# Kernel tuning notes

Hardware: AMD Instinct MI355X
Metric: run time of the kernel (lower is better)

Reference implementation:

```python
import jax, jax.numpy as jnp
import numpy as np
from jax import lax

B, K = 16, 10
C_IN, C_OUT = 32, 64
H_IN, W_IN = 32, 32
KS, STRIDE, PAD = 3, 1, 1
H_OUT = (H_IN + 2 * PAD - KS) // STRIDE + 1
W_OUT = (W_IN + 2 * PAD - KS) // STRIDE + 1


def setup_inputs() -> dict:
    key = jax.random.key(0)
    k1, k2, k3 = jax.random.split(key, 3)
    x = jax.random.normal(k1, (B, K, C_IN, H_IN, W_IN), dtype=jnp.float32)
    # init_local (non-mono, non-first): std = 1/sqrt(0.5 * in_ch * k^2)
    std = 1.0 / np.sqrt(0.5 * C_IN * KS ** 2)
    weight = jax.random.normal(k2, (H_OUT, W_OUT, C_OUT, C_IN, KS, KS), dtype=jnp.float32) * std
    bias = jax.random.normal(k3, (K, C_OUT, H_OUT, W_OUT), dtype=jnp.float32) * 0.01
    return {"x": x, "weight": weight, "bias": bias}


def reference(x, weight, bias):
    # x: [B, K, C_in, H, W] -> merge batch and category dims
    b, k = x.shape[:2]
    xr = x.reshape((b * k,) + x.shape[2:])  # [BK, C_in, H, W]
    # Extract all kxk patches in one fused op: [BK, C_in*KS*KS, h_out, w_out]
    # feature dim ordered (c, kh, kw) -- matches weight layout [o, i, kh, kw].
    patches = lax.conv_general_dilated_patches(
        xr, filter_shape=(KS, KS), window_strides=(STRIDE, STRIDE),
        padding=[(PAD, PAD), (PAD, PAD)])
    w2 = weight.reshape(H_OUT, W_OUT, C_OUT, C_IN * KS * KS)  # [i, j, o, f]
    # Per-pixel unshared contraction (block-diagonal batched GEMM)
    out = jnp.einsum('bfij,ijof->boij', patches, w2)  # [BK, C_out, h_out, w_out]
    out = out.reshape(b, k, C_OUT, H_OUT, W_OUT)
    return out + bias[None]
```

## Files before the change

### kernel.cpp

```cpp
#include <hip/hip_runtime.h>


#define HW    32
#define CIN   32
#define COUT  64
#define FDIM  288
#define FPAD  296
#define NBK   160
#define HP    34
#define PLANE (NBK * CIN)

using f32x4  = __attribute__((ext_vector_type(4))) float;
using bf16x8 = __attribute__((ext_vector_type(8))) short;
using s16x4  = __attribute__((ext_vector_type(4))) short;

static __device__ inline unsigned short f2bf(float f) {
    unsigned u = __float_as_uint(f);
    u += 0x7FFFu + ((u >> 16) & 1u);
    return (unsigned short)(u >> 16);
}
static constexpr size_t XC_BYTES = (size_t)HP * HP * PLANE * 2;
static constexpr size_t CO_BYTES = (size_t)1024 * COUT * NBK * 2;

__global__ __launch_bounds__(256) void hz_kernel(short* __restrict__ xc)
{
    const int id = blockIdx.x;
    int h, w;
    if (id < 34)      { h = 0;  w = id; }
    else if (id < 68) { h = 33; w = id - 34; }
    else { const int e = id - 68; h = 1 + (e >> 1); w = (e & 1) * 33; }
    uint2* p = reinterpret_cast<uint2*>(xc + (size_t)(h * HP + w) * PLANE);
    const uint2 z = {0u, 0u};
#pragma unroll
    for (int r = 0; r < 5; ++r)
        p[threadIdx.x + r * 256] = z;
}

__global__ __launch_bounds__(256) void t1_kernel(
    const float* __restrict__ x, short* __restrict__ xc)
{
    __shared__ short tile[HW][36];
    const int bid = blockIdx.x;
    const int bk  = bid >> 5;
    const int h   = bid & 31;
    const int tid = threadIdx.x;
    {
        const int c  = tid >> 3;
        const int w4 = (tid & 7) * 4;
        const float4 v = *reinterpret_cast<const float4*>(
            x + (size_t)(bk * 32 + c) * 1024 + h * 32 + w4);
        tile[w4 + 0][c] = (short)f2bf(v.x);
        tile[w4 + 1][c] = (short)f2bf(v.y);
        tile[w4 + 2][c] = (short)f2bf(v.z);
        tile[w4 + 3][c] = (short)f2bf(v.w);
    }
    __syncthreads();
    {
        const int w  = tid >> 3;
        const int cq = tid & 7;
        const uint2 pk = *reinterpret_cast<const uint2*>(&tile[w][cq * 4]);
        *reinterpret_cast<uint2*>(
            xc + (size_t)((h + 1) * HP + (w + 1)) * PLANE + bk * CIN + cq * 4) = pk;
    }
}

__global__ __launch_bounds__(512) void local2d_main_kernel(
    const short* __restrict__ xc,
    const float* __restrict__ w,
    short* __restrict__ co)
{
    __shared__ short Wl[COUT * FPAD];

    const int hb  = blockIdx.x;
    const int lb  = (hb & 7) * 128 + (hb >> 3);
    const int i   = lb >> 5;
    const int j   = lb & 31;
    const int pix = i * HW + j;
    const int tid = threadIdx.x;

    {
        const float* wp = w + (size_t)pix * (COUT * FDIM);
        float4 wv[9];
#pragma unroll
        for (int p = 0; p < 9; ++p) {
            const int g  = tid + p * 512;
            const int o  = g / 72;
            const int f4 = (g - o * 72) * 4;
            wv[p] = *reinterpret_cast<const float4*>(wp + o * FDIM + f4);
        }
#pragma unroll
        for (int p = 0; p < 9; ++p) {
            const int g  = tid + p * 512;
            const int o  = g / 72;
            const int f4 = (g - o * 72) * 4;
            const float vv[4] = {wv[p].x, wv[p].y, wv[p].z, wv[p].w};
            short* wrow = &Wl[o * FPAD];
#pragma unroll
            for (int e = 0; e < 4; ++e) {
                const int f    = f4 + e;
                const int c    = f / 9;
                const int cell = f - c * 9;
                wrow[cell * 32 + c] = (short)f2bf(vv[e]);
            }
        }
    }
    __syncthreads();

    const int wave = tid >> 6;
    const int lane = tid & 63;
    const int nt   = wave & 3;
    const int mh   = wave >> 2;
    const int l15  = lane & 15;
    const int lg8  = (lane >> 4) * 8;

    f32x4 acc[5];
#pragma unroll
    for (int mt = 0; mt < 5; ++mt)
#pragma unroll
        for (int r = 0; r < 4; ++r) acc[mt][r] = 0.f;

    const short* bp = &Wl[(nt * 16 + l15) * FPAD + lg8];
    const short* ab = xc + (size_t)(i * HP + j) * PLANE
                         + (mh * 80 + l15) * CIN + lg8;

    bf16x8 abuf[2][5];
#pragma unroll
    for (int mt = 0; mt < 5; ++mt)
        abuf[0][mt] = *reinterpret_cast<const bf16x8*>(ab + mt * 16 * CIN);

#pragma unroll
    for (int kc = 0; kc < 9; ++kc) {
        const int cur = kc & 1;
        if (kc < 8) {
            const int kn  = kc + 1;
            const int off = ((kn / 3) * HP + (kn % 3)) * PLANE;
#pragma unroll
            for (int mt = 0; mt < 5; ++mt)
                abuf[cur ^ 1][mt] =
                    *reinterpret_cast<const bf16x8*>(ab + off + mt * 16 * CIN);
        }
        const bf16x8 b = *reinterpret_cast<const bf16x8*>(bp + kc * 32);
#pragma unroll
        for (int mt = 0; mt < 5; ++mt)
            acc[mt] = __builtin_amdgcn_mfma_f32_16x16x32_bf16(
                abuf[cur][mt], b, acc[mt], 0, 0, 0);
    }

    const int o = nt * 16 + l15;
#pragma unroll
    for (int mt = 0; mt < 5; ++mt) {
        const int bk0 = mh * 80 + mt * 16 + (lane >> 4) * 4;
        s16x4 s;
        s.x = (short)f2bf(acc[mt][0]); s.y = (short)f2bf(acc[mt][1]);
        s.z = (short)f2bf(acc[mt][2]); s.w = (short)f2bf(acc[mt][3]);
        *reinterpret_cast<s16x4*>(co + ((size_t)pix * COUT + o) * NBK + bk0) = s;
    }
}

__global__ __launch_bounds__(256) void t2_kernel(
    const short* __restrict__ co,
    const float* __restrict__ bias,
    float* __restrict__ out)
{
    __shared__ short tl[32][36];
    const int b    = blockIdx.x;
    const int o    = b & 63;
    const int rest = b >> 6;
    const int bkT  = rest % 5;
    const int pixT = rest / 5;
    const int tid  = threadIdx.x;
    {
        const int p  = tid >> 3;
        const int bq = tid & 7;
        const int pix = pixT * 32 + p;
        const s16x4 v = *reinterpret_cast<const s16x4*>(
            co + ((size_t)pix * COUT + o) * NBK + bkT * 32 + bq * 4);
        *reinterpret_cast<s16x4*>(&tl[p][bq * 4]) = v;
    }
    __syncthreads();
    {
        const int bb = tid >> 3;
        const int pq = tid & 7;
        const int bk = bkT * 32 + bb;
        const int k  = bk % 10;
        const size_t pbase = (size_t)pixT * 32 + pq * 4;
        const float4 bv = *reinterpret_cast<const float4*>(
            bias + ((size_t)(k * COUT + o) << 10) + pbase);
        float4 r;
        r.x = __uint_as_float(((unsigned)(unsigned short)tl[pq * 4 + 0][bb]) << 16) + bv.x;
        r.y = __uint_as_float(((unsigned)(unsigned short)tl[pq * 4 + 1][bb]) << 16) + bv.y;
        r.z = __uint_as_float(((unsigned)(unsigned short)tl[pq * 4 + 2][bb]) << 16) + bv.z;
        r.w = __uint_as_float(((unsigned)(unsigned short)tl[pq * 4 + 3][bb]) << 16) + bv.w;
        *reinterpret_cast<float4*>(out + ((size_t)(bk * COUT + o) << 10) + pbase) = r;
    }
}

__global__ __launch_bounds__(256) void xpose_kernel(
    const float* __restrict__ x, short* __restrict__ xc)
{
    __shared__ short tile[HW][36];
    const int bid = blockIdx.x;
    const int bk  = bid >> 5;
    const int h   = bid & 31;
    const int tid = threadIdx.x;
    {
        const int c  = tid >> 3;
        const int w4 = (tid & 7) * 4;
        const float4 v = *reinterpret_cast<const float4*>(
            x + (size_t)(bk * 32 + c) * 1024 + h * 32 + w4);
        tile[w4 + 0][c] = (short)f2bf(v.x);
        tile[w4 + 1][c] = (short)f2bf(v.y);
        tile[w4 + 2][c] = (short)f2bf(v.z);
        tile[w4 + 3][c] = (short)f2bf(v.w);
    }
    __syncthreads();
    {
        const int w  = tid >> 3;
        const int cq = tid & 7;
        const uint2 pk = *reinterpret_cast<const uint2*>(&tile[w][cq * 4]);
        *reinterpret_cast<uint2*>(
            xc + ((size_t)(bk * 1024 + h * 32 + w) * 32 + cq * 4)) = pk;
    }
}

__global__ __launch_bounds__(512, 4) void local2d_mfma2_kernel(
    const short* __restrict__ xc,
    const float* __restrict__ w,
    const float* __restrict__ bias,
    float* __restrict__ out)
{
    __shared__ short Wl[COUT * FPAD];
    const int hb  = blockIdx.x;
    const int lb  = (hb & 7) * 128 + (hb >> 3);
    const int i   = lb >> 5;
    const int j   = lb & 31;
    const int pix = i * HW + j;
    const int tid = threadIdx.x;
    {
        const float* wp = w + (size_t)pix * (COUT * FDIM);
#pragma unroll
        for (int p = 0; p < 9; ++p) {
            const int g  = tid + p * 512;
            const int o  = g / 72;
            const int f4 = (g - o * 72) * 4;
            const float4 v = *reinterpret_cast<const float4*>(wp + o * FDIM + f4);
            const float vv[4] = {v.x, v.y, v.z, v.w};
            short* wrow = &Wl[o * FPAD];
#pragma unroll
            for (int e = 0; e < 4; ++e) {
                const int f    = f4 + e;
                const int c    = f / 9;
                const int cell = f - c * 9;
                wrow[cell * 32 + c] = (short)f2bf(vv[e]);
            }
        }
    }
    __syncthreads();
    const int wave = tid >> 6;
    const int lane = tid & 63;
    const int nt   = wave & 3;
    const int mh   = wave >> 2;
    const int l15  = lane & 15;
    const int lg8  = (lane >> 4) * 8;
    f32x4 acc[5];
#pragma unroll
    for (int mt = 0; mt < 5; ++mt)
#pragma unroll
        for (int r = 0; r < 4; ++r) acc[mt][r] = 0.f;
    const short* xb[5];
#pragma unroll
    for (int mt = 0; mt < 5; ++mt) {
        const int bk = mh * 80 + mt * 16 + l15;
        xb[mt] = xc + (size_t)bk * (HW * HW * CIN) + lg8;
    }
    const short* bp = &Wl[(nt * 16 + l15) * FPAD + lg8];
#pragma unroll
    for (int kc = 0; kc < 9; ++kc) {
        const int kh = kc / 3;
        const int kw = kc - kh * 3;
        const int ih = i - 1 + kh;
        const int jw = j - 1 + kw;
        if ((unsigned)ih >= (unsigned)HW || (unsigned)jw >= (unsigned)HW)
            continue;
        const bf16x8 b = *reinterpret_cast<const bf16x8*>(bp + kc * 32);
        const int xoff = (ih * HW + jw) * CIN;
#pragma unroll
        for (int mt = 0; mt < 5; ++mt) {
            const bf16x8 a = *reinterpret_cast<const bf16x8*>(xb[mt] + xoff);
            acc[mt] = __builtin_amdgcn_mfma_f32_16x16x32_bf16(a, b, acc[mt], 0, 0, 0);
        }
    }
    const int o  = nt * 16 + l15;
    const int r0 = (lane >> 4) * 4;
#pragma unroll
    for (int mt = 0; mt < 5; ++mt) {
        const int bk0 = mh * 80 + mt * 16 + r0;
#pragma unroll
        for (int r = 0; r < 4; ++r) {
            const int bk = bk0 + r;
            const int k  = bk % 10;
            out[((size_t)(bk * COUT + o) << 10) + pix] =
                acc[mt][r] + bias[((size_t)(k * COUT + o) << 10) + pix];
        }
    }
}

extern "C" void kernel_launch(void* const* d_in, const int* in_sizes, int n_in,
                              void* d_out, int out_size, void* d_ws, size_t ws_size,
                              hipStream_t stream) {
    const float* x    = (const float*)d_in[0];
    const float* w    = (const float*)d_in[1];
    const float* bias = (const float*)d_in[2];
    float* out        = (float*)d_out;

    if (ws_size >= XC_BYTES + CO_BYTES) {
        short* xc = (short*)d_ws;
        short* co = (short*)((char*)d_ws + XC_BYTES);
        hipLaunchKernelGGL(hz_kernel, dim3(132), dim3(256), 0, stream, xc);
        hipLaunchKernelGGL(t1_kernel, dim3(5120), dim3(256), 0, stream, x, xc);
        hipLaunchKernelGGL(local2d_main_kernel, dim3(1024), dim3(512), 0, stream,
                           xc, w, co);
        hipLaunchKernelGGL(t2_kernel, dim3(10240), dim3(256), 0, stream,
                           co, bias, out);
    } else {
        short* xc = (short*)d_ws;
        hipLaunchKernelGGL(xpose_kernel, dim3(5120), dim3(256), 0, stream, x, xc);
        hipLaunchKernelGGL(local2d_mfma2_kernel, dim3(1024), dim3(512), 0, stream,
                           xc, w, bias, out);
    }
}
```

Measured before the change: 60.78 us.

## Process four adjacent pixels per block with LDS-staged, swizzled input reuse

The main kernel now handles a row strip of four output pixels per block instead of one. The overlapping 3x3 input neighbourhoods are staged once into LDS through global_load_lds, in a rotating buffer of column slots. The next pixel's weights are prefetched into registers while the current pixel computes, and the t1 layout is XOR-swizzled so the LDS A-fragment reads avoid bank conflicts. This is meant to cut redundant global reads of the shared input columns and to hide the weight-load latency. In exchange the grid drops to 256 blocks, which lowers parallelism on a large GPU, and each block now uses much more LDS.

```diff
diff --git a/kernel.cpp b/kernel.cpp
--- a/kernel.cpp
+++ b/kernel.cpp
@@ -9,6 +9,8 @@
 #define NBK   160
 #define HP    34
 #define PLANE (NBK * CIN)
+#define SLOT_SH (3 * PLANE)
+#define WOFF  (4 * SLOT_SH)
 
 using f32x4  = __attribute__((ext_vector_type(4))) float;
 using bf16x8 = __attribute__((ext_vector_type(8))) short;
@@ -18,6 +20,11 @@
     unsigned u = __float_as_uint(f);
     u += 0x7FFFu + ((u >> 16) & 1u);
     return (unsigned short)(u >> 16);
+}
+static __device__ inline void gl_lds16(const short* src, short* dst) {
+    __builtin_amdgcn_global_load_lds(
+        (const __attribute__((address_space(1))) unsigned int*)src,
+        (__attribute__((address_space(3))) unsigned int*)dst, 16, 0, 0);
 }
 static constexpr size_t XC_BYTES = (size_t)HP * HP * PLANE * 2;
 static constexpr size_t CO_BYTES = (size_t)1024 * COUT * NBK * 2;
@@ -59,8 +66,9 @@
         const int w  = tid >> 3;
         const int cq = tid & 7;
         const uint2 pk = *reinterpret_cast<const uint2*>(&tile[w][cq * 4]);
+        const int sidx = bk * 32 + ((cq * 4) ^ (((bk >> 1) & 3) << 3));
         *reinterpret_cast<uint2*>(
-            xc + (size_t)((h + 1) * HP + (w + 1)) * PLANE + bk * CIN + cq * 4) = pk;
+            xc + (size_t)((h + 1) * HP + (w + 1)) * PLANE + sidx) = pk;
     }
 }
 
@@ -69,92 +77,129 @@
     const float* __restrict__ w,
     short* __restrict__ co)
 {
-    __shared__ short Wl[COUT * FPAD];
-
-    const int hb  = blockIdx.x;
-    const int lb  = (hb & 7) * 128 + (hb >> 3);
-    const int i   = lb >> 5;
-    const int j   = lb & 31;
-    const int pix = i * HW + j;
+    __shared__ __align__(1024) short Sl[WOFF + COUT * FPAD];
+
+    const int hb = blockIdx.x;
+    const int lb = (hb & 7) * 32 + (hb >> 3);
+    const int i  = lb >> 3;
+    const int jt = lb & 7;
+    const int j0 = jt * 4;
     const int tid = threadIdx.x;
-
-    {
-        const float* wp = w + (size_t)pix * (COUT * FDIM);
-        float4 wv[9];
-#pragma unroll
-        for (int p = 0; p < 9; ++p) {
-            const int g  = tid + p * 512;
-            const int o  = g / 72;
-            const int f4 = (g - o * 72) * 4;
-            wv[p] = *reinterpret_cast<const float4*>(wp + o * FDIM + f4);
-        }
-#pragma unroll
-        for (int p = 0; p < 9; ++p) {
-            const int g  = tid + p * 512;
-            const int o  = g / 72;
-            const int f4 = (g - o * 72) * 4;
-            const float vv[4] = {wv[p].x, wv[p].y, wv[p].z, wv[p].w};
-            short* wrow = &Wl[o * FPAD];
-#pragma unroll
-            for (int e = 0; e < 4; ++e) {
-                const int f    = f4 + e;
-                const int c    = f / 9;
-                const int cell = f - c * 9;
-                wrow[cell * 32 + c] = (short)f2bf(vv[e]);
-            }
-        }
-    }
-    __syncthreads();
 
     const int wave = tid >> 6;
     const int lane = tid & 63;
     const int nt   = wave & 3;
     const int mh   = wave >> 2;
     const int l15  = lane & 15;
-    const int lg8  = (lane >> 4) * 8;
-
-    f32x4 acc[5];
-#pragma unroll
-    for (int mt = 0; mt < 5; ++mt)
-#pragma unroll
-        for (int r = 0; r < 4; ++r) acc[mt][r] = 0.f;
-
-    const short* bp = &Wl[(nt * 16 + l15) * FPAD + lg8];
-    const short* ab = xc + (size_t)(i * HP + j) * PLANE
-                         + (mh * 80 + l15) * CIN + lg8;
-
-    bf16x8 abuf[2][5];
-#pragma unroll
-    for (int mt = 0; mt < 5; ++mt)
-        abuf[0][mt] = *reinterpret_cast<const bf16x8*>(ab + mt * 16 * CIN);
-
-#pragma unroll
-    for (int kc = 0; kc < 9; ++kc) {
-        const int cur = kc & 1;
-        if (kc < 8) {
-            const int kn  = kc + 1;
-            const int off = ((kn / 3) * HP + (kn % 3)) * PLANE;
-#pragma unroll
-            for (int mt = 0; mt < 5; ++mt)
-                abuf[cur ^ 1][mt] =
-                    *reinterpret_cast<const bf16x8*>(ab + off + mt * 16 * CIN);
-        }
-        const bf16x8 b = *reinterpret_cast<const bf16x8*>(bp + kc * 32);
-#pragma unroll
-        for (int mt = 0; mt < 5; ++mt)
-            acc[mt] = __builtin_amdgcn_mfma_f32_16x16x32_bf16(
-                abuf[cur][mt], b, acc[mt], 0, 0, 0);
-    }
-
-    const int o = nt * 16 + l15;
+    const int lg   = lane >> 4;
+    const int lg8  = lg * 8;
+
+    short* WL = Sl + WOFF;
+
+    int rowbyte[5];
 #pragma unroll
     for (int mt = 0; mt < 5; ++mt) {
-        const int bk0 = mh * 80 + mt * 16 + (lane >> 4) * 4;
-        s16x4 s;
-        s.x = (short)f2bf(acc[mt][0]); s.y = (short)f2bf(acc[mt][1]);
-        s.z = (short)f2bf(acc[mt][2]); s.w = (short)f2bf(acc[mt][3]);
-        *reinterpret_cast<s16x4*>(co + ((size_t)pix * COUT + o) * NBK + bk0) = s;
-    }
+        const int bk = mh * 80 + mt * 16 + l15;
+        rowbyte[mt] = (bk * 64 + lg * 16) ^ (((bk >> 1) & 3) << 4);
+    }
+
+    float4 wv[9];
+#define WLOAD(pp) {                                                        \
+        const float* wp = w + (size_t)((i * 32) + j0 + (pp)) * (COUT * FDIM); \
+        _Pragma("unroll")                                                  \
+        for (int q = 0; q < 9; ++q) {                                      \
+            const int g  = tid + q * 512;                                  \
+            const int o2 = g / 72;                                         \
+            const int f4 = (g - o2 * 72) * 4;                              \
+            wv[q] = *reinterpret_cast<const float4*>(wp + o2 * FDIM + f4); \
+        } }
+
+    WLOAD(0)
+    {
+#pragma unroll
+        for (int r = 0; r < 15; ++r) {
+            const int u   = tid + r * 512;
+            const int s   = u / 1920;
+            const int rem = u - s * 1920;
+            const int pl  = rem / 640;
+            const int cu  = rem - pl * 640;
+            const short* src = xc + (size_t)((i + pl) * HP + (j0 + s)) * PLANE + cu * 8;
+            gl_lds16(src, Sl + (size_t)u * 8);
+        }
+    }
+
+    const f32x4 z4 = {0.f, 0.f, 0.f, 0.f};
+
+#pragma unroll
+    for (int p = 0; p < 4; ++p) {
+#pragma unroll
+        for (int q = 0; q < 9; ++q) {
+            const int g  = tid + q * 512;
+            const int o2 = g / 72;
+            const int f4 = (g - o2 * 72) * 4;
+            const float vv[4] = {wv[q].x, wv[q].y, wv[q].z, wv[q].w};
+            short* wrow = WL + o2 * FPAD;
+#pragma unroll
+            for (int e = 0; e < 4; ++e) {
+                const int f = f4 + e; const int c = f / 9;
+                const int cell = f - c * 9;
+                wrow[cell * 32 + c] = (short)f2bf(vv[e]);
+            }
+        }
+        __syncthreads();
+
+        if (p < 3) WLOAD(p + 1)
+        if (p == 1 || p == 2) {
+            const int s  = p - 1;
+            const int jw = j0 + 4 + s;
+#pragma unroll
+            for (int r = 0; r < 4; ++r) {
+                const int u = tid + r * 512;
+                if (u < 1920) {
+                    const int pl = u / 640;
+                    const int cu = u - pl * 640;
+                    const short* src = xc + (size_t)((i + pl) * HP + jw) * PLANE + cu * 8;
+                    gl_lds16(src, Sl + (size_t)(s * SLOT_SH) + (size_t)u * 8);
+                }
+            }
+        }
+
+        f32x4 acc0 = z4, acc1 = z4, acc2 = z4, acc3 = z4, acc4 = z4;
+        const short* bp = WL + (nt * 16 + l15) * FPAD + lg8;
+#pragma unroll
+        for (int kc = 0; kc < 9; ++kc) {
+            const int kh   = kc / 3;
+            const int kw   = kc - kh * 3;
+            const int slot = (p + kw) & 3;
+            const char* ab = (const char*)Sl + slot * (SLOT_SH * 2) + kh * (PLANE * 2);
+            const bf16x8 b = *reinterpret_cast<const bf16x8*>(bp + kc * 32);
+            const bf16x8 a0 = *reinterpret_cast<const bf16x8*>(ab + rowbyte[0]);
+            const bf16x8 a1 = *reinterpret_cast<const bf16x8*>(ab + rowbyte[1]);
+            const bf16x8 a2 = *reinterpret_cast<const bf16x8*>(ab + rowbyte[2]);
+            const bf16x8 a3 = *reinterpret_cast<const bf16x8*>(ab + rowbyte[3]);
+            const bf16x8 a4 = *reinterpret_cast<const bf16x8*>(ab + rowbyte[4]);
+            acc0 = __builtin_amdgcn_mfma_f32_16x16x32_bf16(a0, b, acc0, 0, 0, 0);
+            acc1 = __builtin_amdgcn_mfma_f32_16x16x32_bf16(a1, b, acc1, 0, 0, 0);
+            acc2 = __builtin_amdgcn_mfma_f32_16x16x32_bf16(a2, b, acc2, 0, 0, 0);
+            acc3 = __builtin_amdgcn_mfma_f32_16x16x32_bf16(a3, b, acc3, 0, 0, 0);
+            acc4 = __builtin_amdgcn_mfma_f32_16x16x32_bf16(a4, b, acc4, 0, 0, 0);
+        }
+
+        {
+            const int pix = i * 32 + j0 + p;
+            const int o3  = nt * 16 + l15;
+            const size_t cb = ((size_t)pix * COUT + o3) * NBK + mh * 80 + lg * 4;
+#define STORE1(a, mt) { s16x4 s_;                                          \
+            s_.x = (short)f2bf(a[0]); s_.y = (short)f2bf(a[1]);            \
+            s_.z = (short)f2bf(a[2]); s_.w = (short)f2bf(a[3]);            \
+            *reinterpret_cast<s16x4*>(co + cb + (mt) * 16) = s_; }
+            STORE1(acc0, 0) STORE1(acc1, 1) STORE1(acc2, 2)
+            STORE1(acc3, 3) STORE1(acc4, 4)
+#undef STORE1
+        }
+        __syncthreads();
+    }
+#undef WLOAD
 }
 
 __global__ __launch_bounds__(256) void t2_kernel(
@@ -318,7 +363,7 @@
         short* co = (short*)((char*)d_ws + XC_BYTES);
         hipLaunchKernelGGL(hz_kernel, dim3(132), dim3(256), 0, stream, xc);
         hipLaunchKernelGGL(t1_kernel, dim3(5120), dim3(256), 0, stream, x, xc);
-        hipLaunchKernelGGL(local2d_main_kernel, dim3(1024), dim3(512), 0, stream,
+        hipLaunchKernelGGL(local2d_main_kernel, dim3(256), dim3(512), 0, stream,
                            xc, w, co);
         hipLaunchKernelGGL(t2_kernel, dim3(10240), dim3(256), 0, stream,
                            co, bias, out);
```

Measured after the change: 52.44 us. 1.16x faster.

## Load per-pixel weights directly into MFMA fragments, 4 pixels per block

Applied to the files above, without the earlier changes.

The main GEMM kernel no longer stages weights through shared memory. Each wave loads its pixel's fp32 weights straight into registers, converts them to bf16 B-fragments and covers all four output-channel tiles, so one pair of waves handles one pixel and a block handles four pixels (256 blocks instead of 1024). This removes the LDS write, the barrier and the bf16 shuffle through shared memory. In exchange, register pressure rises sharply (a 72-float temp array plus 20 accumulators), A-fragment prefetch is dropped, the weight loads are strided and uncoalesced per lane, and fewer blocks run.

```diff
diff --git a/kernel.cpp b/kernel.cpp
--- a/kernel.cpp
+++ b/kernel.cpp
@@ -64,96 +64,90 @@
     }
 }
 
-__global__ __launch_bounds__(512) void local2d_main_kernel(
+__global__ __launch_bounds__(512) void local2d_g_kernel(
     const short* __restrict__ xc,
     const float* __restrict__ w,
     short* __restrict__ co)
 {
-    __shared__ short Wl[COUT * FPAD];
-
     const int hb  = blockIdx.x;
-    const int lb  = (hb & 7) * 128 + (hb >> 3);
-    const int i   = lb >> 5;
-    const int j   = lb & 31;
+    const int i   = hb >> 3;
+    const int jt  = hb & 7;
+    const int tid = threadIdx.x;
+    const int wid = tid >> 6;
+    const int lane = tid & 63;
+    const int p   = wid >> 1;
+    const int mh  = wid & 1;
+    const int j   = jt * 4 + p;
     const int pix = i * HW + j;
-    const int tid = threadIdx.x;
-
-    {
-        const float* wp = w + (size_t)pix * (COUT * FDIM);
-        float4 wv[9];
-#pragma unroll
-        for (int p = 0; p < 9; ++p) {
-            const int g  = tid + p * 512;
-            const int o  = g / 72;
-            const int f4 = (g - o * 72) * 4;
-            wv[p] = *reinterpret_cast<const float4*>(wp + o * FDIM + f4);
-        }
-#pragma unroll
-        for (int p = 0; p < 9; ++p) {
-            const int g  = tid + p * 512;
-            const int o  = g / 72;
-            const int f4 = (g - o * 72) * 4;
-            const float vv[4] = {wv[p].x, wv[p].y, wv[p].z, wv[p].w};
-            short* wrow = &Wl[o * FPAD];
-#pragma unroll
-            for (int e = 0; e < 4; ++e) {
-                const int f    = f4 + e;
-                const int c    = f / 9;
-                const int cell = f - c * 9;
-                wrow[cell * 32 + c] = (short)f2bf(vv[e]);
+    const int l15 = lane & 15;
+    const int lg  = lane >> 4;
+    const int lg8 = lg * 8;
+
+    const short* abase = xc + ((size_t)i * HP + j) * PLANE
+                            + (mh * 80 + l15) * CIN + lg8;
+
+    f32x4 acc[5][4];
+#pragma unroll
+    for (int mt = 0; mt < 5; ++mt)
+#pragma unroll
+        for (int nt = 0; nt < 4; ++nt)
+#pragma unroll
+            for (int r = 0; r < 4; ++r) acc[mt][nt][r] = 0.f;
+
+#pragma unroll
+    for (int g = 0; g < 2; ++g) {
+        bf16x8 wfr[2][9];
+#pragma unroll
+        for (int ntl = 0; ntl < 2; ++ntl) {
+            const int nt = g * 2 + ntl;
+            const float* q = w + ((size_t)pix * COUT + nt * 16 + l15) * FDIM
+                               + lg8 * 9;
+            float t[72];
+#pragma unroll
+            for (int r = 0; r < 18; ++r)
+                *reinterpret_cast<float4*>(&t[r * 4]) =
+                    *reinterpret_cast<const float4*>(q + r * 4);
+#pragma unroll
+            for (int kc = 0; kc < 9; ++kc) {
+                bf16x8 f;
+#pragma unroll
+                for (int e = 0; e < 8; ++e)
+                    f[e] = (short)f2bf(t[e * 9 + kc]);
+                wfr[ntl][kc] = f;
             }
         }
-    }
-    __syncthreads();
-
-    const int wave = tid >> 6;
-    const int lane = tid & 63;
-    const int nt   = wave & 3;
-    const int mh   = wave >> 2;
-    const int l15  = lane & 15;
-    const int lg8  = (lane >> 4) * 8;
-
-    f32x4 acc[5];
-#pragma unroll
-    for (int mt = 0; mt < 5; ++mt)
-#pragma unroll
-        for (int r = 0; r < 4; ++r) acc[mt][r] = 0.f;
-
-    const short* bp = &Wl[(nt * 16 + l15) * FPAD + lg8];
-    const short* ab = xc + (size_t)(i * HP + j) * PLANE
-                         + (mh * 80 + l15) * CIN + lg8;
-
-    bf16x8 abuf[2][5];
-#pragma unroll
-    for (int mt = 0; mt < 5; ++mt)
-        abuf[0][mt] = *reinterpret_cast<const bf16x8*>(ab + mt * 16 * CIN);
-
-#pragma unroll
-    for (int kc = 0; kc < 9; ++kc) {
-        const int cur = kc & 1;
-        if (kc < 8) {
-            const int kn  = kc + 1;
-            const int off = ((kn / 3) * HP + (kn % 3)) * PLANE;
+
+#pragma unroll
+        for (int kc = 0; kc < 9; ++kc) {
+            const int kh = kc / 3;
+            const int kw = kc - kh * 3;
+            const short* ap = abase + (kh * HP + kw) * PLANE;
+            bf16x8 afr[5];
 #pragma unroll
             for (int mt = 0; mt < 5; ++mt)
-                abuf[cur ^ 1][mt] =
-                    *reinterpret_cast<const bf16x8*>(ab + off + mt * 16 * CIN);
-        }
-        const bf16x8 b = *reinterpret_cast<const bf16x8*>(bp + kc * 32);
-#pragma unroll
-        for (int mt = 0; mt < 5; ++mt)
-            acc[mt] = __builtin_amdgcn_mfma_f32_16x16x32_bf16(
-                abuf[cur][mt], b, acc[mt], 0, 0, 0);
-    }
-
-    const int o = nt * 16 + l15;
-#pragma unroll
-    for (int mt = 0; mt < 5; ++mt) {
-        const int bk0 = mh * 80 + mt * 16 + (lane >> 4) * 4;
-        s16x4 s;
-        s.x = (short)f2bf(acc[mt][0]); s.y = (short)f2bf(acc[mt][1]);
-        s.z = (short)f2bf(acc[mt][2]); s.w = (short)f2bf(acc[mt][3]);
-        *reinterpret_cast<s16x4*>(co + ((size_t)pix * COUT + o) * NBK + bk0) = s;
+                afr[mt] = *reinterpret_cast<const bf16x8*>(ap + mt * 16 * CIN);
+#pragma unroll
+            for (int ntl = 0; ntl < 2; ++ntl) {
+                const int nt = g * 2 + ntl;
+#pragma unroll
+                for (int mt = 0; mt < 5; ++mt)
+                    acc[mt][nt] = __builtin_amdgcn_mfma_f32_16x16x32_bf16(
+                        afr[mt], wfr[ntl][kc], acc[mt][nt], 0, 0, 0);
+            }
+        }
+    }
+
+#pragma unroll
+    for (int nt = 0; nt < 4; ++nt) {
+        const int o = nt * 16 + l15;
+        const size_t cb = ((size_t)pix * COUT + o) * NBK + mh * 80 + lg * 4;
+#pragma unroll
+        for (int mt = 0; mt < 5; ++mt) {
+            s16x4 s;
+            s.x = (short)f2bf(acc[mt][nt][0]); s.y = (short)f2bf(acc[mt][nt][1]);
+            s.z = (short)f2bf(acc[mt][nt][2]); s.w = (short)f2bf(acc[mt][nt][3]);
+            *reinterpret_cast<s16x4*>(co + cb + mt * 16) = s;
+        }
     }
 }
 
@@ -318,7 +312,7 @@
         short* co = (short*)((char*)d_ws + XC_BYTES);
         hipLaunchKernelGGL(hz_kernel, dim3(132), dim3(256), 0, stream, xc);
         hipLaunchKernelGGL(t1_kernel, dim3(5120), dim3(256), 0, stream, x, xc);
-        hipLaunchKernelGGL(local2d_main_kernel, dim3(1024), dim3(512), 0, stream,
+        hipLaunchKernelGGL(local2d_g_kernel, dim3(256), dim3(512), 0, stream,
                            xc, w, co);
         hipLaunchKernelGGL(t2_kernel, dim3(10240), dim3(256), 0, stream,
                            co, bias, out);
```

Result: slower. 107.2 us (+76.3%).
